# Optimization experiments

Hardware: AMD Instinct MI355X
Metric: run time of the kernel (lower is better)

The kernel has to match this reference:

```python
import jax, jax.numpy as jnp
import numpy as np

HEADS = 8
DIM_HEAD = 64
INNER = HEADS * DIM_HEAD  # 512
QUERY_DIM = 1024
CONTEXT_DIM = 768
OUT_DIM = 1024


def setup_inputs() -> dict:
    key = jax.random.key(0)
    ks = jax.random.split(key, 7)
    B, Nq, Nk = 2, 4096, 4096
    s = 0.02
    return {
        "x": jax.random.normal(ks[0], (B, Nq, QUERY_DIM), dtype=jnp.float32),
        "context": jax.random.normal(ks[1], (B, Nk, CONTEXT_DIM), dtype=jnp.float32),
        "w_q": jax.random.normal(ks[2], (QUERY_DIM, INNER), dtype=jnp.float32) * s,
        "w_k": jax.random.normal(ks[3], (CONTEXT_DIM, INNER), dtype=jnp.float32) * s,
        "w_v": jax.random.normal(ks[4], (CONTEXT_DIM, INNER), dtype=jnp.float32) * s,
        "w_out": jax.random.normal(ks[5], (INNER, OUT_DIM), dtype=jnp.float32) * s,
        "b_out": jax.random.normal(ks[6], (OUT_DIM,), dtype=jnp.float32) * s,
    }


def reference(x, context, w_q, w_k, w_v, w_out, b_out):
    h, d = HEADS, DIM_HEAD
    scale = d ** (-0.5)
    B, Nq, _ = x.shape
    Nk = context.shape[1]
    # projections (no bias)
    q = x @ w_q            # [B, Nq, h*d]
    k = context @ w_k      # [B, Nk, h*d]
    v = context @ w_v      # [B, Nk, h*d]
    # split heads: b n (h d) -> b h n d
    q = q.reshape(B, Nq, h, d).transpose(0, 2, 1, 3)
    k = k.reshape(B, Nk, h, d).transpose(0, 2, 1, 3)
    v = v.reshape(B, Nk, h, d).transpose(0, 2, 1, 3)
    sim = jnp.einsum('bhid,bhjd->bhij', q, k) * scale  # [B, h, Nq, Nk]
    attn = jax.nn.softmax(sim, axis=-1)
    out = jnp.einsum('bhij,bhjd->bhid', attn, v)       # [B, h, Nq, d]
    out = out.transpose(0, 2, 1, 3).reshape(B, Nq, h * d)
    return out @ w_out + b_out  # dropout p=0 -> identity
```

## Files before the change

kernel.cpp:

```cpp
#include <hip/hip_runtime.h>
#include <hip/hip_bf16.h>
#include <stdint.h>

#define HEADS 8
#define DHEAD 64
#define INNER 512
#define QDIM 1024
#define CDIM 768
#define ODIM 1024
#define BATCH 2
#define NQ 4096
#define NKEY 4096

using bf16x8 = __attribute__((ext_vector_type(8))) short;
using f32x4  = __attribute__((ext_vector_type(4))) float;

__device__ __forceinline__ unsigned short f2bf(float x) {
    union { float f; unsigned u; } v; v.f = x;
    unsigned r = v.u + 0x7fffu + ((v.u >> 16) & 1u);
    return (unsigned short)(r >> 16);
}

__device__ __forceinline__ unsigned cvtpk(float a, float b) {
    unsigned r;
    asm("v_cvt_pk_bf16_f32 %0, %1, %2" : "=v"(r) : "v"(a), "v"(b));
    return r;
}

__device__ __forceinline__ float exp2a(float x) {
    float r;
    asm("v_exp_f32 %0, %1" : "=v"(r) : "v"(x));
    return r;
}

typedef const __attribute__((address_space(1))) unsigned int* gptr_t;
typedef __attribute__((address_space(3))) unsigned int* lptr_t;

__device__ __forceinline__ void async16(const void* g, void* l) {
    __builtin_amdgcn_global_load_lds((gptr_t)g, (lptr_t)l, 16, 0, 0);
}

#define SGB __builtin_amdgcn_sched_group_barrier

__global__ void k_convert(const float* __restrict__ in, unsigned short* __restrict__ out, int n4) {
    int i = blockIdx.x * blockDim.x + threadIdx.x;
    int stride = gridDim.x * blockDim.x;
    for (; i < n4; i += stride) {
        float4 v = reinterpret_cast<const float4*>(in)[i];
        ushort4 o;
        o.x = f2bf(v.x); o.y = f2bf(v.y); o.z = f2bf(v.z); o.w = f2bf(v.w);
        reinterpret_cast<ushort4*>(out)[i] = o;
    }
}

__global__ void k_transpose_bf16(const float* __restrict__ in, unsigned short* __restrict__ out,
                                 int R, int C) {
    __shared__ float tile[32][33];
    int c0 = blockIdx.x * 32, r0 = blockIdx.y * 32;
    int tx = threadIdx.x, ty = threadIdx.y;
    #pragma unroll
    for (int i = 0; i < 32; i += 8)
        tile[ty + i][tx] = in[(size_t)(r0 + ty + i) * C + c0 + tx];
    __syncthreads();
    #pragma unroll
    for (int i = 0; i < 32; i += 8)
        out[(size_t)(c0 + ty + i) * R + r0 + tx] = f2bf(tile[tx][ty + i]);
}

template <int OUTMODE>
__global__ __launch_bounds__(256) void k_gemm(const unsigned short* __restrict__ A,
                                              const unsigned short* __restrict__ BT,
                                              void* __restrict__ Cout,
                                              const float* __restrict__ bias,
                                              int M, int N, int Kd, float scale) {
    __shared__ alignas(16) unsigned short As[2][128 * 64];
    __shared__ alignas(16) unsigned short Bs[2][64 * 64];
    const int tid = threadIdx.x, lane = tid & 63, w = tid >> 6;
    const int g = lane >> 4, ql = lane & 15;
    const int m0 = blockIdx.x * 128, n0 = blockIdx.y * 64;
    const int wm = (w >> 1) * 64, wn = (w & 1) * 32;
    f32x4 acc[4][2] = {};

    const int srow = tid >> 3;
    const int schunk = ((tid & 7) ^ (srow & 7)) << 3;
    const unsigned short* gA = A + (size_t)(m0 + srow) * Kd + schunk;
    const unsigned short* gB = BT + (size_t)(n0 + srow) * Kd + schunk;

    auto stage = [&](int buf, int kt) {
        char* lA = (char*)As[buf] + (w << 10);
        char* lB = (char*)Bs[buf] + (w << 10);
        async16(gA + kt, lA);
        async16(gA + kt + (size_t)32 * Kd, lA + 4096);
        async16(gA + kt + (size_t)64 * Kd, lA + 8192);
        async16(gA + kt + (size_t)96 * Kd, lA + 12288);
        async16(gB + kt, lB);
        async16(gB + kt + (size_t)32 * Kd, lB + 4096);
    };

#define GCOMP(BUF) { \
        _Pragma("unroll") \
        for (int kk = 0; kk < 2; kk++) { \
            bf16x8 af[4], bfr[2]; \
            _Pragma("unroll") \
            for (int mi = 0; mi < 4; mi++) { \
                int r = wm + mi * 16 + ql; \
                af[mi] = *(const bf16x8*)((const char*)As[BUF] + r * 128 + ((kk * 64 + (g << 4)) ^ ((r & 7) << 4))); \
            } \
            _Pragma("unroll") \
            for (int ni = 0; ni < 2; ni++) { \
                int r = wn + ni * 16 + ql; \
                bfr[ni] = *(const bf16x8*)((const char*)Bs[BUF] + r * 128 + ((kk * 64 + (g << 4)) ^ ((r & 7) << 4))); \
            } \
            _Pragma("unroll") \
            for (int mi = 0; mi < 4; mi++) \
                _Pragma("unroll") \
                for (int ni = 0; ni < 2; ni++) \
                    acc[mi][ni] = __builtin_amdgcn_mfma_f32_16x16x32_bf16(af[mi], bfr[ni], acc[mi][ni], 0, 0, 0); \
        } \
    }

    stage(0, 0);
    for (int kt = 0; kt < Kd; kt += 128) {
        asm volatile("s_waitcnt vmcnt(0)" ::: "memory");
        __builtin_amdgcn_s_barrier();
        __builtin_amdgcn_sched_barrier(0);
        if (kt + 64 < Kd) stage(1, kt + 64);
        GCOMP(0);
        asm volatile("s_waitcnt vmcnt(0)" ::: "memory");
        __builtin_amdgcn_s_barrier();
        __builtin_amdgcn_sched_barrier(0);
        if (kt + 128 < Kd) stage(0, kt + 128);
        GCOMP(1);
    }
#undef GCOMP

    #pragma unroll
    for (int mi = 0; mi < 4; mi++) {
        #pragma unroll
        for (int ni = 0; ni < 2; ni++) {
            int col = n0 + wn + ni * 16 + ql;
            #pragma unroll
            for (int j = 0; j < 4; j++) {
                int row = m0 + wm + mi * 16 + (g << 2) + j;
                float v = acc[mi][ni][j] * scale;
                if (OUTMODE == 0) {
                    ((unsigned short*)Cout)[(size_t)row * N + col] = f2bf(v);
                } else {
                    ((float*)Cout)[(size_t)row * N + col] = v + bias[col];
                }
            }
        }
    }
}

__global__ __launch_bounds__(256, 2) void k_attn(const unsigned short* __restrict__ Q,
                                                 const unsigned short* __restrict__ K,
                                                 const unsigned short* __restrict__ Vt,
                                                 unsigned short* __restrict__ P0,
                                                 unsigned short* __restrict__ P1,
                                                 float* __restrict__ L0,
                                                 float* __restrict__ L1) {
    __shared__ alignas(16) unsigned short Ks[2][64 * 64];
    __shared__ alignas(16) unsigned short Vs[2][64 * 64];
    const int tid = threadIdx.x, lane = tid & 63, w = tid >> 6;
    const int g = lane >> 4, ql = lane & 15;
    const int q0 = blockIdx.x * 128;
    const int b = blockIdx.y >> 3, h = blockIdx.y & 7;
    const int half = blockIdx.z;
    const int kbase = half * (NKEY / 2);
    unsigned short* Pout = half ? P1 : P0;
    float* Lout = half ? L1 : L0;

    const unsigned short* qp = Q + (size_t)(b * NQ + q0 + w * 32 + ql) * INNER
                                 + h * DHEAD + (g << 3);
    bf16x8 qf00 = *(const bf16x8*)qp;
    bf16x8 qf01 = *(const bf16x8*)(qp + 32);
    bf16x8 qf10 = *(const bf16x8*)(qp + 16 * INNER);
    bf16x8 qf11 = *(const bf16x8*)(qp + 16 * INNER + 32);

    f32x4 po0[4] = {}, po1[4] = {};
    float ls0 = 0.f, ls1 = 0.f;
    const f32x4 zero4 = {0.f, 0.f, 0.f, 0.f};

    const int m0 = tid >> 3;
    const int rho0 = ((m0 & 28) << 1) + (m0 & 3);
    const int srcslot = ((tid & 7) ^ (m0 & 7)) << 3;
    const unsigned short* gK = K + (size_t)(b * NKEY + kbase + rho0) * INNER + h * DHEAD + srcslot;
    const unsigned short* gV = Vt + (size_t)(h * DHEAD + m0) * (BATCH * NKEY) + b * NKEY + kbase + srcslot;

    auto stageK = [&](int nb, int kt) {
        char* lK = (char*)Ks[nb] + (w << 10);
        async16(gK + (size_t)kt * INNER, lK);
        async16(gK + (size_t)(kt + 4) * INNER, lK + 4096);
    };
    auto stageV = [&](int nb, int kt) {
        char* lV = (char*)Vs[nb] + (w << 10);
        async16(gV + kt, lV);
        async16(gV + kt + (size_t)32 * (BATCH * NKEY), lV + 4096);
    };

    union pfu { bf16x8 v; unsigned u[4]; };

#define SMCHUNK(MI, SC0, SC1, pA, pB, lsa, lsb) { \
        float a0 = exp2a(SC0[MI][0]), a1 = exp2a(SC0[MI][1]); \
        float a2 = exp2a(SC0[MI][2]), a3 = exp2a(SC0[MI][3]); \
        float b0 = exp2a(SC1[MI][0]), b1 = exp2a(SC1[MI][1]); \
        float b2 = exp2a(SC1[MI][2]), b3 = exp2a(SC1[MI][3]); \
        lsa += (a0 + a1) + (a2 + a3); \
        lsb += (b0 + b1) + (b2 + b3); \
        pA[MI & 1].u[(MI >> 1) * 2 + 0] = cvtpk(a0, a1); \
        pA[MI & 1].u[(MI >> 1) * 2 + 1] = cvtpk(a2, a3); \
        pB[MI & 1].u[(MI >> 1) * 2 + 0] = cvtpk(b0, b1); \
        pB[MI & 1].u[(MI >> 1) * 2 + 1] = cvtpk(b2, b3); \
    }

#define QKM(KBUF, S0, S1) { \
        const char* Kb_ = (const char*)(KBUF); \
        _Pragma("unroll") \
        for (int mi = 0; mi < 4; mi++) { \
            int rK = mi * 16 + ql; \
            int sw = (rK & 7) << 4; \
            bf16x8 kf0 = *(const bf16x8*)(Kb_ + rK * 128 + ((g << 4) ^ sw)); \
            bf16x8 kf1 = *(const bf16x8*)(Kb_ + rK * 128 + ((64 + (g << 4)) ^ sw)); \
            S0[mi] = __builtin_amdgcn_mfma_f32_16x16x32_bf16(kf0, qf00, zero4, 0, 0, 0); \
            S0[mi] = __builtin_amdgcn_mfma_f32_16x16x32_bf16(kf1, qf01, S0[mi], 0, 0, 0); \
            S1[mi] = __builtin_amdgcn_mfma_f32_16x16x32_bf16(kf0, qf10, zero4, 0, 0, 0); \
            S1[mi] = __builtin_amdgcn_mfma_f32_16x16x32_bf16(kf1, qf11, S1[mi], 0, 0, 0); \
        } \
    }

#define PVM(VBUF, pA, pB) { \
        const char* Vb_ = (const char*)(VBUF); \
        bf16x8 vf0[4], vf1[4]; \
        _Pragma("unroll") \
        for (int mi = 0; mi < 4; mi++) { \
            int rV = mi * 16 + ql; \
            int sw = (rV & 7) << 4; \
            vf0[mi] = *(const bf16x8*)(Vb_ + rV * 128 + ((g << 4) ^ sw)); \
            vf1[mi] = *(const bf16x8*)(Vb_ + rV * 128 + ((64 + (g << 4)) ^ sw)); \
        } \
        _Pragma("unroll") \
        for (int mi = 0; mi < 4; mi++) { \
            po0[mi] = __builtin_amdgcn_mfma_f32_16x16x32_bf16(vf0[mi], pA[0].v, po0[mi], 0, 0, 0); \
            po0[mi] = __builtin_amdgcn_mfma_f32_16x16x32_bf16(vf1[mi], pA[1].v, po0[mi], 0, 0, 0); \
            po1[mi] = __builtin_amdgcn_mfma_f32_16x16x32_bf16(vf0[mi], pB[0].v, po1[mi], 0, 0, 0); \
            po1[mi] = __builtin_amdgcn_mfma_f32_16x16x32_bf16(vf1[mi], pB[1].v, po1[mi], 0, 0, 0); \
        } \
    }

#define ABODY(T, CUR, SC0, SC1, SN0, SN1, DO_K, DO_V) { \
        asm volatile("s_waitcnt vmcnt(0)" ::: "memory"); \
        __builtin_amdgcn_s_barrier(); \
        __builtin_amdgcn_sched_barrier(0); \
        if (DO_K) stageK(CUR, (T + 2) * 64); \
        if (DO_V) stageV(CUR ^ 1, (T + 1) * 64); \
        const char* Kb_ = (const char*)Ks[CUR ^ 1]; \
        bf16x8 kf0[4], kf1[4]; \
        _Pragma("unroll") \
        for (int mi = 0; mi < 4; mi++) { \
            int rK = mi * 16 + ql; \
            int sw = (rK & 7) << 4; \
            kf0[mi] = *(const bf16x8*)(Kb_ + rK * 128 + ((g << 4) ^ sw)); \
            kf1[mi] = *(const bf16x8*)(Kb_ + rK * 128 + ((64 + (g << 4)) ^ sw)); \
        } \
        __builtin_amdgcn_sched_group_barrier(0x100, 8, 0); \
        pfu pA[2], pB[2]; \
        float lsa = 0.f, lsb = 0.f; \
        _Pragma("unroll") \
        for (int mi = 0; mi < 4; mi++) { \
            SMCHUNK(mi, SC0, SC1, pA, pB, lsa, lsb); \
            __builtin_amdgcn_sched_group_barrier(0x2, 18, 0); \
            SN0[mi] = __builtin_amdgcn_mfma_f32_16x16x32_bf16(kf0[mi], qf00, zero4, 0, 0, 0); \
            SN0[mi] = __builtin_amdgcn_mfma_f32_16x16x32_bf16(kf1[mi], qf01, SN0[mi], 0, 0, 0); \
            SN1[mi] = __builtin_amdgcn_mfma_f32_16x16x32_bf16(kf0[mi], qf10, zero4, 0, 0, 0); \
            SN1[mi] = __builtin_amdgcn_mfma_f32_16x16x32_bf16(kf1[mi], qf11, SN1[mi], 0, 0, 0); \
            __builtin_amdgcn_sched_group_barrier(0x8, 4, 0); \
        } \
        ls0 += lsa; ls1 += lsb; \
        __builtin_amdgcn_s_setprio(1); \
        PVM(Vs[CUR], pA, pB); \
        __builtin_amdgcn_sched_group_barrier(0x100, 8, 0); \
        __builtin_amdgcn_sched_group_barrier(0x8, 16, 0); \
        __builtin_amdgcn_s_setprio(0); \
    }

    f32x4 sE0[4], sE1[4], sO0[4], sO1[4];

    stageK(0, 0); stageV(0, 0); stageK(1, 64);
    asm volatile("s_waitcnt vmcnt(2)" ::: "memory");
    __builtin_amdgcn_s_barrier();
    __builtin_amdgcn_sched_barrier(0);
    QKM(Ks[0], sE0, sE1);

    for (int t = 0; t < 30; t += 2) {
        ABODY(t, 0, sE0, sE1, sO0, sO1, 1, 1);
        ABODY(t + 1, 1, sO0, sO1, sE0, sE1, 1, 1);
    }
    ABODY(30, 0, sE0, sE1, sO0, sO1, 0, 1);

    asm volatile("s_waitcnt vmcnt(0)" ::: "memory");
    __builtin_amdgcn_s_barrier();
    __builtin_amdgcn_sched_barrier(0);
    {
        pfu pA[2], pB[2];
        float lsa = 0.f, lsb = 0.f;
        #pragma unroll
        for (int mi = 0; mi < 4; mi++) {
            SMCHUNK(mi, sO0, sO1, pA, pB, lsa, lsb);
        }
        ls0 += lsa; ls1 += lsb;
        PVM(Vs[1], pA, pB);
    }

    ls0 += __shfl_xor(ls0, 16); ls0 += __shfl_xor(ls0, 32);
    ls1 += __shfl_xor(ls1, 16); ls1 += __shfl_xor(ls1, 32);
    const int row0 = b * NQ + q0 + w * 32 + ql;
    unsigned short* pp = Pout + (size_t)row0 * INNER + h * DHEAD + (g << 2);
    #pragma unroll
    for (int mi = 0; mi < 4; mi++) {
        uint2 uu;
        uu.x = cvtpk(po0[mi][0], po0[mi][1]);
        uu.y = cvtpk(po0[mi][2], po0[mi][3]);
        *(uint2*)(pp + mi * 16) = uu;
        uint2 vv;
        vv.x = cvtpk(po1[mi][0], po1[mi][1]);
        vv.y = cvtpk(po1[mi][2], po1[mi][3]);
        *(uint2*)(pp + 16 * INNER + mi * 16) = vv;
    }
    if (g == 0) {
        Lout[(size_t)row0 * HEADS + h] = ls0;
        Lout[(size_t)(row0 + 16) * HEADS + h] = ls1;
    }
#undef ABODY
#undef PVM
#undef QKM
#undef SMCHUNK
}

__global__ __launch_bounds__(256) void k_combine(const unsigned short* __restrict__ P0,
                                                 const unsigned short* __restrict__ P1,
                                                 const float* __restrict__ L0,
                                                 const float* __restrict__ L1,
                                                 unsigned short* __restrict__ O) {
    int idx = blockIdx.x * 256 + threadIdx.x;
    int row = idx >> 6, c8 = idx & 63, h = c8 >> 3;
    float inv = 1.0f / (L0[(size_t)row * HEADS + h] + L1[(size_t)row * HEADS + h]);
    uint4 a = ((const uint4*)P0)[idx];
    uint4 bb = ((const uint4*)P1)[idx];
    uint4 o;
    unsigned* ap = (unsigned*)&a;
    unsigned* bp = (unsigned*)&bb;
    unsigned* op = (unsigned*)&o;
    #pragma unroll
    for (int i = 0; i < 4; i++) {
        union { unsigned u; float f; } alo, ahi, blo, bhi;
        alo.u = ap[i] << 16;          ahi.u = ap[i] & 0xffff0000u;
        blo.u = bp[i] << 16;          bhi.u = bp[i] & 0xffff0000u;
        op[i] = cvtpk((alo.f + blo.f) * inv, (ahi.f + bhi.f) * inv);
    }
    ((uint4*)O)[idx] = o;
}

extern "C" void kernel_launch(void* const* d_in, const int* in_sizes, int n_in,
                              void* d_out, int out_size, void* d_ws, size_t ws_size,
                              hipStream_t stream) {
    const float* x     = (const float*)d_in[0];
    const float* ctx   = (const float*)d_in[1];
    const float* w_q   = (const float*)d_in[2];
    const float* w_k   = (const float*)d_in[3];
    const float* w_v   = (const float*)d_in[4];
    const float* w_out = (const float*)d_in[5];
    const float* b_out = (const float*)d_in[6];
    float* out = (float*)d_out;

    char* ws = (char*)d_ws;
    size_t off = 0;
    auto alloc = [&](size_t bytes) { void* p = ws + off; off += (bytes + 255) & ~(size_t)255; return p; };
    unsigned short* xb  = (unsigned short*)alloc((size_t)BATCH * NQ * QDIM * 2);
    unsigned short* cb  = (unsigned short*)alloc((size_t)BATCH * NKEY * CDIM * 2);
    unsigned short* wqT = (unsigned short*)alloc((size_t)INNER * QDIM * 2);
    unsigned short* wkT = (unsigned short*)alloc((size_t)INNER * CDIM * 2);
    unsigned short* wvT = (unsigned short*)alloc((size_t)INNER * CDIM * 2);
    unsigned short* woT = (unsigned short*)alloc((size_t)ODIM * INNER * 2);
    unsigned short* Qb  = (unsigned short*)alloc((size_t)BATCH * NQ * INNER * 2);
    unsigned short* Kb  = (unsigned short*)alloc((size_t)BATCH * NKEY * INNER * 2);
    unsigned short* Vtb = (unsigned short*)alloc((size_t)INNER * BATCH * NKEY * 2);
    unsigned short* Ob  = (unsigned short*)alloc((size_t)BATCH * NQ * INNER * 2);
    float* L0 = (float*)alloc((size_t)BATCH * NQ * HEADS * 4);
    float* L1 = (float*)alloc((size_t)BATCH * NQ * HEADS * 4);
    unsigned short* P0 = xb;
    unsigned short* P1 = cb;

    k_convert<<<2048, 256, 0, stream>>>(x, xb, BATCH * NQ * QDIM / 4);
    k_convert<<<2048, 256, 0, stream>>>(ctx, cb, BATCH * NKEY * CDIM / 4);

    dim3 tb(32, 8);
    k_transpose_bf16<<<dim3(INNER / 32, QDIM / 32), tb, 0, stream>>>(w_q, wqT, QDIM, INNER);
    k_transpose_bf16<<<dim3(INNER / 32, CDIM / 32), tb, 0, stream>>>(w_k, wkT, CDIM, INNER);
    k_transpose_bf16<<<dim3(INNER / 32, CDIM / 32), tb, 0, stream>>>(w_v, wvT, CDIM, INNER);
    k_transpose_bf16<<<dim3(ODIM / 32, INNER / 32), tb, 0, stream>>>(w_out, woT, INNER, ODIM);

    k_gemm<0><<<dim3(8192 / 128, 512 / 64), 256, 0, stream>>>(xb, wqT, Qb, nullptr, 8192, 512, 1024, 0.1803368801111204f);
    k_gemm<0><<<dim3(8192 / 128, 512 / 64), 256, 0, stream>>>(cb, wkT, Kb, nullptr, 8192, 512, 768, 1.0f);
    k_gemm<0><<<dim3(512 / 128, 8192 / 64), 256, 0, stream>>>(wvT, cb, Vtb, nullptr, 512, 8192, 768, 1.0f);

    k_attn<<<dim3(NQ / 128, BATCH * HEADS, 2), 256, 0, stream>>>(Qb, Kb, Vtb, P0, P1, L0, L1);
    k_combine<<<(BATCH * NQ * INNER / 8) / 256, 256, 0, stream>>>(P0, P1, L0, L1, Ob);

    k_gemm<1><<<dim3(8192 / 128, 1024 / 64), 256, 0, stream>>>(Ob, woT, out, b_out, 8192, 1024, 512, 1.0f);
}
```

Measured before the change: 162.3 us.

## Rework attention kernel to 32x32 MFMA tiles with 256-query blocks

The attention kernel now uses 32x32x16 bf16 MFMA instead of 16x16x32. Each wave handles 64 query rows, so a block covers 256 queries and the grid is halved. The old software pipeline, which overlapped next-tile QK with the current softmax and used sched_group_barrier hints, is replaced by a simpler double-buffered loop that stages K and V together and computes QK, exp and PV on the same tile. The goal is to reuse each K/V tile across more queries and cut LDS reads per FLOP. In exchange it raises register pressure (16-float accumulators, more Q fragments), loses the QK/softmax overlap, and halves the number of blocks, which leaves fewer waves to hide latency.

Result: slower. 187.0 us (+15.3%).

```diff
diff --git a/kernel.cpp b/kernel.cpp
--- a/kernel.cpp
+++ b/kernel.cpp
@@ -14,6 +14,7 @@
 
 using bf16x8 = __attribute__((ext_vector_type(8))) short;
 using f32x4  = __attribute__((ext_vector_type(4))) float;
+using f32x16 = __attribute__((ext_vector_type(16))) float;
 
 __device__ __forceinline__ unsigned short f2bf(float x) {
     union { float f; unsigned u; } v; v.f = x;
@@ -39,8 +40,6 @@
 __device__ __forceinline__ void async16(const void* g, void* l) {
     __builtin_amdgcn_global_load_lds((gptr_t)g, (lptr_t)l, 16, 0, 0);
 }
-
-#define SGB __builtin_amdgcn_sched_group_barrier
 
 __global__ void k_convert(const float* __restrict__ in, unsigned short* __restrict__ out, int n4) {
     int i = blockIdx.x * blockDim.x + threadIdx.x;
@@ -163,178 +162,139 @@
     __shared__ alignas(16) unsigned short Ks[2][64 * 64];
     __shared__ alignas(16) unsigned short Vs[2][64 * 64];
     const int tid = threadIdx.x, lane = tid & 63, w = tid >> 6;
-    const int g = lane >> 4, ql = lane & 15;
-    const int q0 = blockIdx.x * 128;
+    const int q32 = lane & 31, hi = lane >> 5;
+    const int q0 = blockIdx.x * 256;
     const int b = blockIdx.y >> 3, h = blockIdx.y & 7;
     const int half = blockIdx.z;
     const int kbase = half * (NKEY / 2);
     unsigned short* Pout = half ? P1 : P0;
     float* Lout = half ? L1 : L0;
 
-    const unsigned short* qp = Q + (size_t)(b * NQ + q0 + w * 32 + ql) * INNER
-                                 + h * DHEAD + (g << 3);
-    bf16x8 qf00 = *(const bf16x8*)qp;
-    bf16x8 qf01 = *(const bf16x8*)(qp + 32);
-    bf16x8 qf10 = *(const bf16x8*)(qp + 16 * INNER);
-    bf16x8 qf11 = *(const bf16x8*)(qp + 16 * INNER + 32);
-
-    f32x4 po0[4] = {}, po1[4] = {};
+    const unsigned short* qbase = Q + (size_t)(b * NQ + q0 + w * 64 + q32) * INNER
+                                    + h * DHEAD + hi * 8;
+    bf16x8 qf[2][4];
+    #pragma unroll
+    for (int qt = 0; qt < 2; qt++)
+        #pragma unroll
+        for (int j = 0; j < 4; j++)
+            qf[qt][j] = *(const bf16x8*)(qbase + qt * 32 * INNER + j * 16);
+
+    f32x16 po[2][2] = {};
     float ls0 = 0.f, ls1 = 0.f;
-    const f32x4 zero4 = {0.f, 0.f, 0.f, 0.f};
-
-    const int m0 = tid >> 3;
-    const int rho0 = ((m0 & 28) << 1) + (m0 & 3);
-    const int srcslot = ((tid & 7) ^ (m0 & 7)) << 3;
-    const unsigned short* gK = K + (size_t)(b * NKEY + kbase + rho0) * INNER + h * DHEAD + srcslot;
-    const unsigned short* gV = Vt + (size_t)(h * DHEAD + m0) * (BATCH * NKEY) + b * NKEY + kbase + srcslot;
-
-    auto stageK = [&](int nb, int kt) {
+    const f32x16 z16 = {};
+
+    const int m = tid >> 3;
+    const int rho = (m & ~12) | ((m & 4) << 1) | ((m & 8) >> 1);
+    const int srcc = ((tid & 7) ^ (m & 7)) << 3;
+    const unsigned short* gK = K + (size_t)(b * NKEY + kbase + rho) * INNER + h * DHEAD + srcc;
+    const unsigned short* gV = Vt + (size_t)(h * DHEAD + m) * (BATCH * NKEY) + b * NKEY + kbase + srcc;
+
+    auto stage = [&](int nb, int t64) {
         char* lK = (char*)Ks[nb] + (w << 10);
-        async16(gK + (size_t)kt * INNER, lK);
-        async16(gK + (size_t)(kt + 4) * INNER, lK + 4096);
+        char* lV = (char*)Vs[nb] + (w << 10);
+        const int ko = t64 * 64;
+        async16(gK + (size_t)ko * INNER, lK);
+        async16(gK + (size_t)(ko + 32) * INNER, lK + 4096);
+        async16(gV + ko, lV);
+        async16(gV + ko + (size_t)32 * (BATCH * NKEY), lV + 4096);
     };
-    auto stageV = [&](int nb, int kt) {
-        char* lV = (char*)Vs[nb] + (w << 10);
-        async16(gV + kt, lV);
-        async16(gV + kt + (size_t)32 * (BATCH * NKEY), lV + 4096);
-    };
 
     union pfu { bf16x8 v; unsigned u[4]; };
 
-#define SMCHUNK(MI, SC0, SC1, pA, pB, lsa, lsb) { \
-        float a0 = exp2a(SC0[MI][0]), a1 = exp2a(SC0[MI][1]); \
-        float a2 = exp2a(SC0[MI][2]), a3 = exp2a(SC0[MI][3]); \
-        float b0 = exp2a(SC1[MI][0]), b1 = exp2a(SC1[MI][1]); \
-        float b2 = exp2a(SC1[MI][2]), b3 = exp2a(SC1[MI][3]); \
-        lsa += (a0 + a1) + (a2 + a3); \
-        lsb += (b0 + b1) + (b2 + b3); \
-        pA[MI & 1].u[(MI >> 1) * 2 + 0] = cvtpk(a0, a1); \
-        pA[MI & 1].u[(MI >> 1) * 2 + 1] = cvtpk(a2, a3); \
-        pB[MI & 1].u[(MI >> 1) * 2 + 0] = cvtpk(b0, b1); \
-        pB[MI & 1].u[(MI >> 1) * 2 + 1] = cvtpk(b2, b3); \
-    }
-
-#define QKM(KBUF, S0, S1) { \
-        const char* Kb_ = (const char*)(KBUF); \
-        _Pragma("unroll") \
-        for (int mi = 0; mi < 4; mi++) { \
-            int rK = mi * 16 + ql; \
-            int sw = (rK & 7) << 4; \
-            bf16x8 kf0 = *(const bf16x8*)(Kb_ + rK * 128 + ((g << 4) ^ sw)); \
-            bf16x8 kf1 = *(const bf16x8*)(Kb_ + rK * 128 + ((64 + (g << 4)) ^ sw)); \
-            S0[mi] = __builtin_amdgcn_mfma_f32_16x16x32_bf16(kf0, qf00, zero4, 0, 0, 0); \
-            S0[mi] = __builtin_amdgcn_mfma_f32_16x16x32_bf16(kf1, qf01, S0[mi], 0, 0, 0); \
-            S1[mi] = __builtin_amdgcn_mfma_f32_16x16x32_bf16(kf0, qf10, zero4, 0, 0, 0); \
-            S1[mi] = __builtin_amdgcn_mfma_f32_16x16x32_bf16(kf1, qf11, S1[mi], 0, 0, 0); \
-        } \
-    }
-
-#define PVM(VBUF, pA, pB) { \
-        const char* Vb_ = (const char*)(VBUF); \
-        bf16x8 vf0[4], vf1[4]; \
-        _Pragma("unroll") \
-        for (int mi = 0; mi < 4; mi++) { \
-            int rV = mi * 16 + ql; \
-            int sw = (rV & 7) << 4; \
-            vf0[mi] = *(const bf16x8*)(Vb_ + rV * 128 + ((g << 4) ^ sw)); \
-            vf1[mi] = *(const bf16x8*)(Vb_ + rV * 128 + ((64 + (g << 4)) ^ sw)); \
-        } \
-        _Pragma("unroll") \
-        for (int mi = 0; mi < 4; mi++) { \
-            po0[mi] = __builtin_amdgcn_mfma_f32_16x16x32_bf16(vf0[mi], pA[0].v, po0[mi], 0, 0, 0); \
-            po0[mi] = __builtin_amdgcn_mfma_f32_16x16x32_bf16(vf1[mi], pA[1].v, po0[mi], 0, 0, 0); \
-            po1[mi] = __builtin_amdgcn_mfma_f32_16x16x32_bf16(vf0[mi], pB[0].v, po1[mi], 0, 0, 0); \
-            po1[mi] = __builtin_amdgcn_mfma_f32_16x16x32_bf16(vf1[mi], pB[1].v, po1[mi], 0, 0, 0); \
-        } \
-    }
-
-#define ABODY(T, CUR, SC0, SC1, SN0, SN1, DO_K, DO_V) { \
+#define ABODY(T, CUR, DOSTAGE) { \
         asm volatile("s_waitcnt vmcnt(0)" ::: "memory"); \
         __builtin_amdgcn_s_barrier(); \
         __builtin_amdgcn_sched_barrier(0); \
-        if (DO_K) stageK(CUR, (T + 2) * 64); \
-        if (DO_V) stageV(CUR ^ 1, (T + 1) * 64); \
-        const char* Kb_ = (const char*)Ks[CUR ^ 1]; \
-        bf16x8 kf0[4], kf1[4]; \
+        if (DOSTAGE) stage(CUR ^ 1, (T) + 1); \
+        const char* Kb_ = (const char*)Ks[CUR]; \
+        const char* Vb_ = (const char*)Vs[CUR]; \
+        f32x16 sc[2][2]; \
+        __builtin_amdgcn_s_setprio(1); \
         _Pragma("unroll") \
-        for (int mi = 0; mi < 4; mi++) { \
-            int rK = mi * 16 + ql; \
-            int sw = (rK & 7) << 4; \
-            kf0[mi] = *(const bf16x8*)(Kb_ + rK * 128 + ((g << 4) ^ sw)); \
-            kf1[mi] = *(const bf16x8*)(Kb_ + rK * 128 + ((64 + (g << 4)) ^ sw)); \
+        for (int r = 0; r < 2; r++) { \
+            int R = r * 32 + q32; \
+            int sw = (R & 7) << 4; \
+            _Pragma("unroll") \
+            for (int j = 0; j < 4; j++) { \
+                bf16x8 kf = *(const bf16x8*)(Kb_ + R * 128 + ((((j * 2 + hi) << 4)) ^ sw)); \
+                if (j == 0) { \
+                    sc[0][r] = __builtin_amdgcn_mfma_f32_32x32x16_bf16(kf, qf[0][0], z16, 0, 0, 0); \
+                    sc[1][r] = __builtin_amdgcn_mfma_f32_32x32x16_bf16(kf, qf[1][0], z16, 0, 0, 0); \
+                } else { \
+                    sc[0][r] = __builtin_amdgcn_mfma_f32_32x32x16_bf16(kf, qf[0][j], sc[0][r], 0, 0, 0); \
+                    sc[1][r] = __builtin_amdgcn_mfma_f32_32x32x16_bf16(kf, qf[1][j], sc[1][r], 0, 0, 0); \
+                } \
+            } \
         } \
-        __builtin_amdgcn_sched_group_barrier(0x100, 8, 0); \
-        pfu pA[2], pB[2]; \
-        float lsa = 0.f, lsb = 0.f; \
+        __builtin_amdgcn_s_setprio(0); \
+        pfu pf[2][2][2]; \
         _Pragma("unroll") \
-        for (int mi = 0; mi < 4; mi++) { \
-            SMCHUNK(mi, SC0, SC1, pA, pB, lsa, lsb); \
-            __builtin_amdgcn_sched_group_barrier(0x2, 18, 0); \
-            SN0[mi] = __builtin_amdgcn_mfma_f32_16x16x32_bf16(kf0[mi], qf00, zero4, 0, 0, 0); \
-            SN0[mi] = __builtin_amdgcn_mfma_f32_16x16x32_bf16(kf1[mi], qf01, SN0[mi], 0, 0, 0); \
-            SN1[mi] = __builtin_amdgcn_mfma_f32_16x16x32_bf16(kf0[mi], qf10, zero4, 0, 0, 0); \
-            SN1[mi] = __builtin_amdgcn_mfma_f32_16x16x32_bf16(kf1[mi], qf11, SN1[mi], 0, 0, 0); \
-            __builtin_amdgcn_sched_group_barrier(0x8, 4, 0); \
+        for (int qt = 0; qt < 2; qt++) { \
+            float acc = 0.f; \
+            _Pragma("unroll") \
+            for (int r = 0; r < 2; r++) { \
+                float p[16]; \
+                _Pragma("unroll") \
+                for (int i = 0; i < 16; i++) p[i] = exp2a(qt ? sc[1][r][i] : sc[0][r][i]); \
+                acc += (((p[0] + p[1]) + (p[2] + p[3])) + ((p[4] + p[5]) + (p[6] + p[7]))) \
+                     + (((p[8] + p[9]) + (p[10] + p[11])) + ((p[12] + p[13]) + (p[14] + p[15]))); \
+                pf[qt][r][0].u[0] = cvtpk(p[0], p[1]);   pf[qt][r][0].u[1] = cvtpk(p[2], p[3]); \
+                pf[qt][r][0].u[2] = cvtpk(p[4], p[5]);   pf[qt][r][0].u[3] = cvtpk(p[6], p[7]); \
+                pf[qt][r][1].u[0] = cvtpk(p[8], p[9]);   pf[qt][r][1].u[1] = cvtpk(p[10], p[11]); \
+                pf[qt][r][1].u[2] = cvtpk(p[12], p[13]); pf[qt][r][1].u[3] = cvtpk(p[14], p[15]); \
+            } \
+            if (qt) ls1 += acc; else ls0 += acc; \
         } \
-        ls0 += lsa; ls1 += lsb; \
         __builtin_amdgcn_s_setprio(1); \
-        PVM(Vs[CUR], pA, pB); \
-        __builtin_amdgcn_sched_group_barrier(0x100, 8, 0); \
-        __builtin_amdgcn_sched_group_barrier(0x8, 16, 0); \
+        _Pragma("unroll") \
+        for (int dt = 0; dt < 2; dt++) { \
+            int R = dt * 32 + q32; \
+            int sw = (R & 7) << 4; \
+            _Pragma("unroll") \
+            for (int r = 0; r < 2; r++) { \
+                _Pragma("unroll") \
+                for (int eo = 0; eo < 2; eo++) { \
+                    int j2 = r * 2 + eo; \
+                    bf16x8 vf = *(const bf16x8*)(Vb_ + R * 128 + ((((j2 * 2 + hi) << 4)) ^ sw)); \
+                    po[dt][0] = __builtin_amdgcn_mfma_f32_32x32x16_bf16(vf, pf[0][r][eo].v, po[dt][0], 0, 0, 0); \
+                    po[dt][1] = __builtin_amdgcn_mfma_f32_32x32x16_bf16(vf, pf[1][r][eo].v, po[dt][1], 0, 0, 0); \
+                } \
+            } \
+        } \
         __builtin_amdgcn_s_setprio(0); \
     }
 
-    f32x4 sE0[4], sE1[4], sO0[4], sO1[4];
-
-    stageK(0, 0); stageV(0, 0); stageK(1, 64);
-    asm volatile("s_waitcnt vmcnt(2)" ::: "memory");
-    __builtin_amdgcn_s_barrier();
-    __builtin_amdgcn_sched_barrier(0);
-    QKM(Ks[0], sE0, sE1);
-
+    stage(0, 0);
     for (int t = 0; t < 30; t += 2) {
-        ABODY(t, 0, sE0, sE1, sO0, sO1, 1, 1);
-        ABODY(t + 1, 1, sO0, sO1, sE0, sE1, 1, 1);
-    }
-    ABODY(30, 0, sE0, sE1, sO0, sO1, 0, 1);
-
-    asm volatile("s_waitcnt vmcnt(0)" ::: "memory");
-    __builtin_amdgcn_s_barrier();
-    __builtin_amdgcn_sched_barrier(0);
-    {
-        pfu pA[2], pB[2];
-        float lsa = 0.f, lsb = 0.f;
+        ABODY(t, 0, 1);
+        ABODY(t + 1, 1, 1);
+    }
+    ABODY(30, 0, 1);
+    ABODY(31, 1, 0);
+
+    ls0 += __shfl_xor(ls0, 32);
+    ls1 += __shfl_xor(ls1, 32);
+    #pragma unroll
+    for (int qt = 0; qt < 2; qt++) {
+        int row = b * NQ + q0 + w * 64 + qt * 32 + q32;
+        unsigned short* pp = Pout + (size_t)row * INNER + h * DHEAD;
         #pragma unroll
-        for (int mi = 0; mi < 4; mi++) {
-            SMCHUNK(mi, sO0, sO1, pA, pB, lsa, lsb);
+        for (int dt = 0; dt < 2; dt++) {
+            #pragma unroll
+            for (int k = 0; k < 4; k++) {
+                uint2 uu;
+                float a0 = qt ? po[dt][1][4 * k + 0] : po[dt][0][4 * k + 0];
+                float a1 = qt ? po[dt][1][4 * k + 1] : po[dt][0][4 * k + 1];
+                float a2 = qt ? po[dt][1][4 * k + 2] : po[dt][0][4 * k + 2];
+                float a3 = qt ? po[dt][1][4 * k + 3] : po[dt][0][4 * k + 3];
+                uu.x = cvtpk(a0, a1);
+                uu.y = cvtpk(a2, a3);
+                *(uint2*)(pp + dt * 32 + k * 8 + hi * 4) = uu;
+            }
         }
-        ls0 += lsa; ls1 += lsb;
-        PVM(Vs[1], pA, pB);
-    }
-
-    ls0 += __shfl_xor(ls0, 16); ls0 += __shfl_xor(ls0, 32);
-    ls1 += __shfl_xor(ls1, 16); ls1 += __shfl_xor(ls1, 32);
-    const int row0 = b * NQ + q0 + w * 32 + ql;
-    unsigned short* pp = Pout + (size_t)row0 * INNER + h * DHEAD + (g << 2);
-    #pragma unroll
-    for (int mi = 0; mi < 4; mi++) {
-        uint2 uu;
-        uu.x = cvtpk(po0[mi][0], po0[mi][1]);
-        uu.y = cvtpk(po0[mi][2], po0[mi][3]);
-        *(uint2*)(pp + mi * 16) = uu;
-        uint2 vv;
-        vv.x = cvtpk(po1[mi][0], po1[mi][1]);
-        vv.y = cvtpk(po1[mi][2], po1[mi][3]);
-        *(uint2*)(pp + 16 * INNER + mi * 16) = vv;
-    }
-    if (g == 0) {
-        Lout[(size_t)row0 * HEADS + h] = ls0;
-        Lout[(size_t)(row0 + 16) * HEADS + h] = ls1;
+        if (hi == 0) Lout[(size_t)row * HEADS + h] = qt ? ls1 : ls0;
     }
 #undef ABODY
-#undef PVM
-#undef QKM
-#undef SMCHUNK
 }
 
 __global__ __launch_bounds__(256) void k_combine(const unsigned short* __restrict__ P0,
@@ -404,7 +364,7 @@
     k_gemm<0><<<dim3(8192 / 128, 512 / 64), 256, 0, stream>>>(cb, wkT, Kb, nullptr, 8192, 512, 768, 1.0f);
     k_gemm<0><<<dim3(512 / 128, 8192 / 64), 256, 0, stream>>>(wvT, cb, Vtb, nullptr, 512, 8192, 768, 1.0f);
 
-    k_attn<<<dim3(NQ / 128, BATCH * HEADS, 2), 256, 0, stream>>>(Qb, Kb, Vtb, P0, P1, L0, L1);
+    k_attn<<<dim3(NQ / 256, BATCH * HEADS, 2), 256, 0, stream>>>(Qb, Kb, Vtb, P0, P1, L0, L1);
     k_combine<<<(BATCH * NQ * INNER / 8) / 256, 256, 0, stream>>>(P0, P1, L0, L1, Ob);
 
     k_gemm<1><<<dim3(8192 / 128, 1024 / 64), 256, 0, stream>>>(Ob, woT, out, b_out, 8192, 1024, 512, 1.0f);
```

## Replace software-pipelined QK/softmax overlap with simple loop and raise occupancy

Applied to the files above, without the earlier changes.

Drops the software-pipelined attention loop, which interleaved the next tile's QK MFMAs with the current tile's exp/softmax under sched_group_barrier hints. Each iteration now runs QK, softmax and PV sequentially on one double-buffered K/V tile, and launch bounds move from 2 to 3 blocks per SIMD. The aim is to cut register pressure (no second set of score accumulators) so more waves can hide latency across wavefronts instead of within one. The cost is that overlap of VALU and MFMA work inside a wave is lost, and the tighter register budget may cause spills.

New measurement: 167.8 us. +3.4%, slower.

```diff
diff --git a/kernel.cpp b/kernel.cpp
--- a/kernel.cpp
+++ b/kernel.cpp
@@ -39,8 +39,6 @@
 __device__ __forceinline__ void async16(const void* g, void* l) {
     __builtin_amdgcn_global_load_lds((gptr_t)g, (lptr_t)l, 16, 0, 0);
 }
-
-#define SGB __builtin_amdgcn_sched_group_barrier
 
 __global__ void k_convert(const float* __restrict__ in, unsigned short* __restrict__ out, int n4) {
     int i = blockIdx.x * blockDim.x + threadIdx.x;
@@ -153,7 +151,7 @@
     }
 }
 
-__global__ __launch_bounds__(256, 2) void k_attn(const unsigned short* __restrict__ Q,
+__global__ __launch_bounds__(256, 3) void k_attn(const unsigned short* __restrict__ Q,
                                                  const unsigned short* __restrict__ K,
                                                  const unsigned short* __restrict__ Vt,
                                                  unsigned short* __restrict__ P0,
@@ -214,102 +212,53 @@
         pB[MI & 1].u[(MI >> 1) * 2 + 1] = cvtpk(b2, b3); \
     }
 
-#define QKM(KBUF, S0, S1) { \
-        const char* Kb_ = (const char*)(KBUF); \
+#define ABODY(T, CUR, DOSTAGE) { \
+        asm volatile("s_waitcnt vmcnt(0)" ::: "memory"); \
+        __builtin_amdgcn_s_barrier(); \
+        __builtin_amdgcn_sched_barrier(0); \
+        if (DOSTAGE) { stageK(CUR ^ 1, (T + 1) * 64); stageV(CUR ^ 1, (T + 1) * 64); } \
+        const char* Kb_ = (const char*)Ks[CUR]; \
+        const char* Vb_ = (const char*)Vs[CUR]; \
+        f32x4 s0[4], s1[4]; \
+        __builtin_amdgcn_s_setprio(1); \
         _Pragma("unroll") \
         for (int mi = 0; mi < 4; mi++) { \
             int rK = mi * 16 + ql; \
             int sw = (rK & 7) << 4; \
             bf16x8 kf0 = *(const bf16x8*)(Kb_ + rK * 128 + ((g << 4) ^ sw)); \
             bf16x8 kf1 = *(const bf16x8*)(Kb_ + rK * 128 + ((64 + (g << 4)) ^ sw)); \
-            S0[mi] = __builtin_amdgcn_mfma_f32_16x16x32_bf16(kf0, qf00, zero4, 0, 0, 0); \
-            S0[mi] = __builtin_amdgcn_mfma_f32_16x16x32_bf16(kf1, qf01, S0[mi], 0, 0, 0); \
-            S1[mi] = __builtin_amdgcn_mfma_f32_16x16x32_bf16(kf0, qf10, zero4, 0, 0, 0); \
-            S1[mi] = __builtin_amdgcn_mfma_f32_16x16x32_bf16(kf1, qf11, S1[mi], 0, 0, 0); \
+            s0[mi] = __builtin_amdgcn_mfma_f32_16x16x32_bf16(kf0, qf00, zero4, 0, 0, 0); \
+            s0[mi] = __builtin_amdgcn_mfma_f32_16x16x32_bf16(kf1, qf01, s0[mi], 0, 0, 0); \
+            s1[mi] = __builtin_amdgcn_mfma_f32_16x16x32_bf16(kf0, qf10, zero4, 0, 0, 0); \
+            s1[mi] = __builtin_amdgcn_mfma_f32_16x16x32_bf16(kf1, qf11, s1[mi], 0, 0, 0); \
         } \
-    }
-
-#define PVM(VBUF, pA, pB) { \
-        const char* Vb_ = (const char*)(VBUF); \
-        bf16x8 vf0[4], vf1[4]; \
+        __builtin_amdgcn_s_setprio(0); \
+        pfu pA[2], pB[2]; \
+        float lsa = 0.f, lsb = 0.f; \
+        _Pragma("unroll") \
+        for (int mi = 0; mi < 4; mi++) { \
+            SMCHUNK(mi, s0, s1, pA, pB, lsa, lsb); \
+        } \
+        ls0 += lsa; ls1 += lsb; \
+        __builtin_amdgcn_s_setprio(1); \
         _Pragma("unroll") \
         for (int mi = 0; mi < 4; mi++) { \
             int rV = mi * 16 + ql; \
             int sw = (rV & 7) << 4; \
-            vf0[mi] = *(const bf16x8*)(Vb_ + rV * 128 + ((g << 4) ^ sw)); \
-            vf1[mi] = *(const bf16x8*)(Vb_ + rV * 128 + ((64 + (g << 4)) ^ sw)); \
+            bf16x8 vf0 = *(const bf16x8*)(Vb_ + rV * 128 + ((g << 4) ^ sw)); \
+            bf16x8 vf1 = *(const bf16x8*)(Vb_ + rV * 128 + ((64 + (g << 4)) ^ sw)); \
+            po0[mi] = __builtin_amdgcn_mfma_f32_16x16x32_bf16(vf0, pA[0].v, po0[mi], 0, 0, 0); \
+            po0[mi] = __builtin_amdgcn_mfma_f32_16x16x32_bf16(vf1, pA[1].v, po0[mi], 0, 0, 0); \
+            po1[mi] = __builtin_amdgcn_mfma_f32_16x16x32_bf16(vf0, pB[0].v, po1[mi], 0, 0, 0); \
+            po1[mi] = __builtin_amdgcn_mfma_f32_16x16x32_bf16(vf1, pB[1].v, po1[mi], 0, 0, 0); \
         } \
-        _Pragma("unroll") \
-        for (int mi = 0; mi < 4; mi++) { \
-            po0[mi] = __builtin_amdgcn_mfma_f32_16x16x32_bf16(vf0[mi], pA[0].v, po0[mi], 0, 0, 0); \
-            po0[mi] = __builtin_amdgcn_mfma_f32_16x16x32_bf16(vf1[mi], pA[1].v, po0[mi], 0, 0, 0); \
-            po1[mi] = __builtin_amdgcn_mfma_f32_16x16x32_bf16(vf0[mi], pB[0].v, po1[mi], 0, 0, 0); \
-            po1[mi] = __builtin_amdgcn_mfma_f32_16x16x32_bf16(vf1[mi], pB[1].v, po1[mi], 0, 0, 0); \
-        } \
-    }
-
-#define ABODY(T, CUR, SC0, SC1, SN0, SN1, DO_K, DO_V) { \
-        asm volatile("s_waitcnt vmcnt(0)" ::: "memory"); \
-        __builtin_amdgcn_s_barrier(); \
-        __builtin_amdgcn_sched_barrier(0); \
-        if (DO_K) stageK(CUR, (T + 2) * 64); \
-        if (DO_V) stageV(CUR ^ 1, (T + 1) * 64); \
-        const char* Kb_ = (const char*)Ks[CUR ^ 1]; \
-        bf16x8 kf0[4], kf1[4]; \
-        _Pragma("unroll") \
-        for (int mi = 0; mi < 4; mi++) { \
-            int rK = mi * 16 + ql; \
-            int sw = (rK & 7) << 4; \
-            kf0[mi] = *(const bf16x8*)(Kb_ + rK * 128 + ((g << 4) ^ sw)); \
-            kf1[mi] = *(const bf16x8*)(Kb_ + rK * 128 + ((64 + (g << 4)) ^ sw)); \
-        } \
-        __builtin_amdgcn_sched_group_barrier(0x100, 8, 0); \
-        pfu pA[2], pB[2]; \
-        float lsa = 0.f, lsb = 0.f; \
-        _Pragma("unroll") \
-        for (int mi = 0; mi < 4; mi++) { \
-            SMCHUNK(mi, SC0, SC1, pA, pB, lsa, lsb); \
-            __builtin_amdgcn_sched_group_barrier(0x2, 18, 0); \
-            SN0[mi] = __builtin_amdgcn_mfma_f32_16x16x32_bf16(kf0[mi], qf00, zero4, 0, 0, 0); \
-            SN0[mi] = __builtin_amdgcn_mfma_f32_16x16x32_bf16(kf1[mi], qf01, SN0[mi], 0, 0, 0); \
-            SN1[mi] = __builtin_amdgcn_mfma_f32_16x16x32_bf16(kf0[mi], qf10, zero4, 0, 0, 0); \
-            SN1[mi] = __builtin_amdgcn_mfma_f32_16x16x32_bf16(kf1[mi], qf11, SN1[mi], 0, 0, 0); \
-            __builtin_amdgcn_sched_group_barrier(0x8, 4, 0); \
-        } \
-        ls0 += lsa; ls1 += lsb; \
-        __builtin_amdgcn_s_setprio(1); \
-        PVM(Vs[CUR], pA, pB); \
-        __builtin_amdgcn_sched_group_barrier(0x100, 8, 0); \
-        __builtin_amdgcn_sched_group_barrier(0x8, 16, 0); \
         __builtin_amdgcn_s_setprio(0); \
     }
 
-    f32x4 sE0[4], sE1[4], sO0[4], sO1[4];
-
-    stageK(0, 0); stageV(0, 0); stageK(1, 64);
-    asm volatile("s_waitcnt vmcnt(2)" ::: "memory");
-    __builtin_amdgcn_s_barrier();
-    __builtin_amdgcn_sched_barrier(0);
-    QKM(Ks[0], sE0, sE1);
-
-    for (int t = 0; t < 30; t += 2) {
-        ABODY(t, 0, sE0, sE1, sO0, sO1, 1, 1);
-        ABODY(t + 1, 1, sO0, sO1, sE0, sE1, 1, 1);
-    }
-    ABODY(30, 0, sE0, sE1, sO0, sO1, 0, 1);
-
-    asm volatile("s_waitcnt vmcnt(0)" ::: "memory");
-    __builtin_amdgcn_s_barrier();
-    __builtin_amdgcn_sched_barrier(0);
-    {
-        pfu pA[2], pB[2];
-        float lsa = 0.f, lsb = 0.f;
-        #pragma unroll
-        for (int mi = 0; mi < 4; mi++) {
-            SMCHUNK(mi, sO0, sO1, pA, pB, lsa, lsb);
-        }
-        ls0 += lsa; ls1 += lsb;
-        PVM(Vs[1], pA, pB);
+    stageK(0, 0); stageV(0, 0);
+    for (int t = 0; t < 32; t += 2) {
+        ABODY(t, 0, 1);
+        ABODY(t + 1, 1, (t + 2 < 32));
     }
 
     ls0 += __shfl_xor(ls0, 16); ls0 += __shfl_xor(ls0, 32);
@@ -332,8 +281,6 @@
         Lout[(size_t)(row0 + 16) * HEADS + h] = ls1;
     }
 #undef ABODY
-#undef PVM
-#undef QKM
 #undef SMCHUNK
 }
 
```
